# Performance work log

Measured on AMD Instinct MI355X. Metric: run time of the kernel, lower is better.

The kernel has to match this reference:

```python
import jax, jax.numpy as jnp
import numpy as np
from jax.ops import segment_sum, segment_max

N = 100000   # nodes
E = 1600000  # edges
B = 256      # graphs
H = 128      # hidden_channels
F_IN = 4     # input_size
EPS = 1e-5


def _graph_norm(x, w, b, ms, batch):
    # PyG GraphNorm: out = w * (x - ms*mean_g) / sqrt(var_g + eps) + b
    cnt = jnp.maximum(segment_sum(jnp.ones((x.shape[0],), x.dtype), batch, num_segments=B), 1.0)
    mean = segment_sum(x, batch, num_segments=B) / cnt[:, None]
    out = x - mean[batch] * ms
    var = segment_sum(out * out, batch, num_segments=B) / cnt[:, None]
    return w * out / jnp.sqrt(var + EPS)[batch] + b


def _gcn(x, W, b, src, dst):
    # GCNConv with self-loops and symmetric normalization (src/dst already include self-loops)
    h = x @ W                                              # [N, H]
    deg = segment_sum(jnp.ones_like(src, dtype=h.dtype), dst, num_segments=N)
    dinv = jax.lax.rsqrt(jnp.maximum(deg, 1.0))
    norm = dinv[src] * dinv[dst]                           # [E+N]
    return segment_sum(norm[:, None] * h[src], dst, num_segments=N) + b


def _seg_softmax(gate, batch):
    gmax = segment_max(gate, batch, num_segments=B)
    e = jnp.exp(gate - gmax[batch])
    den = segment_sum(e, batch, num_segments=B)
    return e / den[batch]


def setup_inputs() -> dict:
    key = jax.random.key(0)
    ks = jax.random.split(key, 16)
    x = jax.random.normal(ks[0], (N, F_IN), jnp.float32)
    edge_index = jax.random.randint(ks[1], (2, E), 0, N, dtype=jnp.int64)
    batch = jnp.sort(jax.random.randint(ks[2], (N,), 0, B, dtype=jnp.int64))
    r = lambda k, shp, fan: jax.random.normal(k, shp, jnp.float32) / np.sqrt(fan)
    inp = {
        "x": x, "edge_index": edge_index, "batch": batch,
        "W1": r(ks[3], (F_IN, H), F_IN), "b1": jnp.zeros((H,), jnp.float32),
        "W2": r(ks[4], (H, H), H), "b2": jnp.zeros((H,), jnp.float32),
        "W3": r(ks[5], (H, H), H), "b3": jnp.zeros((H,), jnp.float32),
        "gn0_w": jnp.ones((F_IN,), jnp.float32), "gn0_b": jnp.zeros((F_IN,), jnp.float32), "gn0_ms": jnp.ones((F_IN,), jnp.float32),
        "gn1_w": jnp.ones((H,), jnp.float32), "gn1_b": jnp.zeros((H,), jnp.float32), "gn1_ms": jnp.ones((H,), jnp.float32),
        "gn2_w": jnp.ones((H,), jnp.float32), "gn2_b": jnp.zeros((H,), jnp.float32), "gn2_ms": jnp.ones((H,), jnp.float32),
        "gn3_w": jnp.ones((H,), jnp.float32), "gn3_b": jnp.zeros((H,), jnp.float32), "gn3_ms": jnp.ones((H,), jnp.float32),
        "g1": r(ks[6], (H, H), H), "gb1": jnp.zeros((H,), jnp.float32),
        "g2": r(ks[7], (H, H), H), "gb2": jnp.zeros((H,), jnp.float32),
        "g3": r(ks[8], (H, 1), H), "gb3": jnp.zeros((1,), jnp.float32),
        "l1": r(ks[9], (H, H), H), "lb1": jnp.zeros((H,), jnp.float32),
        "l2": r(ks[10], (H, H), H), "lb2": jnp.zeros((H,), jnp.float32),
        "l3": r(ks[11], (H, 1), H), "lb3": jnp.zeros((1,), jnp.float32),
    }
    return inp


def reference(x, edge_index, batch, W1, b1, W2, b2, W3, b3,
              gn0_w, gn0_b, gn0_ms, gn1_w, gn1_b, gn1_ms,
              gn2_w, gn2_b, gn2_ms, gn3_w, gn3_b, gn3_ms,
              g1, gb1, g2, gb2, g3, gb3,
              l1, lb1, l2, lb2, l3, lb3):
    loop = jnp.arange(N, dtype=edge_index.dtype)
    src = jnp.concatenate([edge_index[0], loop])
    dst = jnp.concatenate([edge_index[1], loop])

    h = _graph_norm(x, gn0_w, gn0_b, gn0_ms, batch)
    h = _gcn(h, W1, b1, src, dst)
    h = jax.nn.relu(_graph_norm(h, gn1_w, gn1_b, gn1_ms, batch))
    h = _gcn(h, W2, b2, src, dst)
    h = jax.nn.relu(_graph_norm(h, gn2_w, gn2_b, gn2_ms, batch))
    h = _gcn(h, W3, b3, src, dst)
    h = _graph_norm(h, gn3_w, gn3_b, gn3_ms, batch)

    # GlobalAttention: gate_nn -> scalar gate per node, segment softmax, weighted sum
    g = jax.nn.relu(h @ g1 + gb1)
    g = jax.nn.relu(g @ g2 + gb2)
    gate = g @ g3 + gb3                                   # [N, 1]
    attn = _seg_softmax(gate, batch)                      # [N, 1]
    pooled = segment_sum(attn * h, batch, num_segments=B) # [B, H]

    o = jax.nn.relu(pooled @ l1 + lb1)
    o = jax.nn.relu(o @ l2 + lb2)
    return o @ l3 + lb3                                   # [B, 1]
```

## Files before the change

kernel.cpp:

```cpp
#include <hip/hip_runtime.h>
#include <hip/hip_bf16.h>

#define NN 100000
#define NE 1600000
#define NB 256
#define HD 128
#define EPS 1e-5f
#define NBUK 1563
#define EPB 8192
#define NCHK 8

typedef __attribute__((ext_vector_type(8))) short bf16x8v;
typedef __attribute__((ext_vector_type(4))) float f32x4v;

__device__ __forceinline__ float rd_dyn(const void* p, int i, int fflag) {
    if (fflag) {
        unsigned short u = ((const unsigned short*)p)[i];
        return __uint_as_float(((unsigned)u) << 16);
    }
    return ((const float*)p)[i];
}

__device__ __forceinline__ int rd_idx(const int* p, int k, int iflag) {
    return iflag ? p[k] : p[2 * k];
}

__device__ __forceinline__ unsigned short f2bf(float v) {
    __hip_bfloat16 b = __float2bfloat16(v);
    return *(unsigned short*)&b;
}

__device__ __forceinline__ float bflo(unsigned u) { return __uint_as_float(u << 16); }
__device__ __forceinline__ float bfhi(unsigned u) { return __uint_as_float(u & 0xFFFF0000u); }
__device__ __forceinline__ unsigned packbf(float a, float b) {
    return (unsigned)f2bf(a) | ((unsigned)f2bf(b) << 16);
}

__global__ void k_mark7(unsigned short* __restrict__ out, int n) {
    int i = blockIdx.x * blockDim.x + threadIdx.x;
    if (i < n) out[i] = 0x40E0;
}

__global__ void k_init(const unsigned* __restrict__ w, int* __restrict__ flags) {
    if (threadIdx.x == 0 && blockIdx.x == 0) {
        flags[0] = 0;
        flags[1] = (w[0] == 0x3F803F80u) ? 1 : 0;
    }
}

__global__ void k_detect(const int* __restrict__ w, int* __restrict__ iflag, int n) {
    int i = blockIdx.x * blockDim.x + threadIdx.x;
    if (i < n && (i & 1) && w[i] != 0) atomicOr(iflag, 1);
}

struct CvtArgs {
    const void* p[30];
    int n[30];
    int off[30];
};
__global__ void k_cvtf_all(CvtArgs a, float* __restrict__ out, const int* __restrict__ fflagp) {
    int j = blockIdx.y;
    int i = blockIdx.x * blockDim.x + threadIdx.x;
    if (i >= a.n[j]) return;
    out[a.off[j] + i] = rd_dyn(a.p[j], i, *fflagp);
}

__global__ void k_transp(const float* __restrict__ P, int o0, int o1, int o2, int o3,
                         unsigned short* __restrict__ WT) {
    int mat = blockIdx.y;
    int off = mat == 0 ? o0 : mat == 1 ? o1 : mat == 2 ? o2 : o3;
    int i = blockIdx.x * 256 + threadIdx.x;
    int nidx = i >> 7, k = i & 127;
    WT[mat * 16384 + nidx * 128 + k] = f2bf(P[off + k * 128 + nidx]);
}

__global__ void k_start(const int* __restrict__ batch, const int* __restrict__ iflagp,
                        int* __restrict__ start, int* __restrict__ batch32,
                        int* __restrict__ bcnt, int n) {
    int i = blockIdx.x * blockDim.x + threadIdx.x;
    if (i >= n) return;
    if (i < NBUK) bcnt[i] = 0;
    int ifl = *iflagp;
    int b = rd_idx(batch, i, ifl); b = b < 0 ? 0 : (b > NB - 1 ? NB - 1 : b);
    batch32[i] = b;
    int bp;
    if (i == 0) bp = -1;
    else { bp = rd_idx(batch, i - 1, ifl); bp = bp < 0 ? 0 : (bp > NB - 1 ? NB - 1 : bp); }
    for (int g = bp + 1; g <= b; ++g) start[g] = i;
    if (i == n - 1) { for (int g = b + 1; g <= NB; ++g) start[g] = n; }
}

__global__ __launch_bounds__(256) void k_bhist(const int* __restrict__ ei,
                                               const int* __restrict__ iflagp,
                                               int* __restrict__ bcnt, int e) {
    __shared__ int lh[NBUK];
    int ifl = *iflagp;
    for (int b = threadIdx.x; b < NBUK; b += 256) lh[b] = 0;
    __syncthreads();
    int s0 = blockIdx.x * EPB;
    int s1 = s0 + EPB; if (s1 > e) s1 = e;
    for (int i = s0 + threadIdx.x; i < s1; i += 256) {
        int d = rd_idx(ei, NE + i, ifl);
        int s = rd_idx(ei, i, ifl);
        if ((unsigned)d < (unsigned)NN && (unsigned)s < (unsigned)NN)
            atomicAdd(&lh[d >> 6], 1);
    }
    __syncthreads();
    for (int b = threadIdx.x; b < NBUK; b += 256)
        if (lh[b]) atomicAdd(&bcnt[b], lh[b]);
}

__global__ __launch_bounds__(1024) void k_bscan(const int* __restrict__ bcnt,
                                                int* __restrict__ boff,
                                                int* __restrict__ bcur) {
    __shared__ int part[1024];
    int t = threadIdx.x;
    int i0 = t * 2;
    int a = (i0 < NBUK) ? bcnt[i0] : 0;
    int b = (i0 + 1 < NBUK) ? bcnt[i0 + 1] : 0;
    part[t] = a + b;
    __syncthreads();
    for (int off = 1; off < 1024; off <<= 1) {
        int add = (t >= off) ? part[t - off] : 0;
        __syncthreads();
        part[t] += add;
        __syncthreads();
    }
    int base = (t > 0) ? part[t - 1] : 0;
    if (i0 < NBUK) { boff[i0] = base; bcur[i0] = base; }
    if (i0 + 1 < NBUK) { boff[i0 + 1] = base + a; bcur[i0 + 1] = base + a; }
    if (t == 1023) boff[NBUK] = part[1023];
}

__global__ __launch_bounds__(256) void k_bfill(const int* __restrict__ ei,
                                               const int* __restrict__ iflagp,
                                               int* __restrict__ bcur,
                                               unsigned* __restrict__ bkte, int e) {
    __shared__ int lh[NBUK];
    __shared__ int lbase[NBUK];
    int ifl = *iflagp;
    for (int b = threadIdx.x; b < NBUK; b += 256) lh[b] = 0;
    __syncthreads();
    int s0 = blockIdx.x * EPB;
    int s1 = s0 + EPB; if (s1 > e) s1 = e;
    for (int i = s0 + threadIdx.x; i < s1; i += 256) {
        int d = rd_idx(ei, NE + i, ifl);
        int s = rd_idx(ei, i, ifl);
        if ((unsigned)d < (unsigned)NN && (unsigned)s < (unsigned)NN)
            atomicAdd(&lh[d >> 6], 1);
    }
    __syncthreads();
    for (int b = threadIdx.x; b < NBUK; b += 256) {
        int c = lh[b];
        if (c) { lbase[b] = atomicAdd(&bcur[b], c); lh[b] = 0; }
    }
    __syncthreads();
    for (int i = s0 + threadIdx.x; i < s1; i += 256) {
        int d = rd_idx(ei, NE + i, ifl);
        int s = rd_idx(ei, i, ifl);
        if ((unsigned)d < (unsigned)NN && (unsigned)s < (unsigned)NN) {
            int b = d >> 6;
            int li = atomicAdd(&lh[b], 1);
            bkte[lbase[b] + li] = ((unsigned)s << 6) | (unsigned)(d & 63);
        }
    }
}

__global__ __launch_bounds__(256) void k_csrfin(const unsigned* __restrict__ bkte,
                                                const int* __restrict__ boff,
                                                int* __restrict__ rowptr,
                                                float* __restrict__ dinv,
                                                int* __restrict__ esrc) {
    __shared__ int lc[64];
    __shared__ int lcur[64];
    int b = blockIdx.x, t = threadIdx.x;
    int base = b * 64;
    if (t < 64) lc[t] = 0;
    __syncthreads();
    int r0 = boff[b], r1 = boff[b + 1];
    for (int j = r0 + t; j < r1; j += 256)
        atomicAdd(&lc[(int)(bkte[j] & 63u)], 1);
    __syncthreads();
    if (t < 64) {
        int v = lc[t];
        int inc = v;
#pragma unroll
        for (int off = 1; off < 64; off <<= 1) {
            int nv = __shfl_up(inc, off, 64);
            if (t >= off) inc += nv;
        }
        int ex = r0 + inc - v;
        lcur[t] = ex;
        int node = base + t;
        if (node < NN) {
            rowptr[node] = ex;
            dinv[node] = rsqrtf((float)(v + 1));
        }
    }
    if (b == NBUK - 1 && t == 0) rowptr[NN] = boff[NBUK];
    __syncthreads();
    for (int j = r0 + t; j < r1; j += 256) {
        unsigned p = bkte[j];
        int slot = atomicAdd(&lcur[p & 63u], 1);
        esrc[slot] = (int)(p >> 6);
    }
}

__global__ __launch_bounds__(64) void k_gn4(const void* __restrict__ x,
                                            const float* __restrict__ w,
                                            const float* __restrict__ bb,
                                            const float* __restrict__ ms,
                                            const int* __restrict__ start,
                                            const int* __restrict__ fflagp,
                                            float* __restrict__ out) {
    int g = blockIdx.x;
    int s0 = start[g], s1 = start[g + 1];
    if (s1 <= s0) return;
    int ff = *fflagp;
    float cnt = (float)(s1 - s0);
    int t = threadIdx.x;
    int c = t & 3, p = t >> 2;
    __shared__ float reds[64], redq[64];
    float s = 0.f, q = 0.f;
    for (int n = s0 + p; n < s1; n += 16) {
        float v = rd_dyn(x, n * 4 + c, ff);
        s += v; q = fmaf(v, v, q);
    }
    reds[t] = s; redq[t] = q; __syncthreads();
    for (int off = 8; off >= 1; off >>= 1) {
        if (p < off) { reds[t] += reds[t + 4 * off]; redq[t] += redq[t + 4 * off]; }
        __syncthreads();
    }
    float mean = reds[c] / cnt;
    float sq = redq[c] / cnt;
    float sub = mean * ms[c];
    float var = sq - 2.f * sub * mean + sub * sub;
    float scale = w[c] * rsqrtf(var + EPS);
    float bias = bb[c];
    for (int n = s0 + p; n < s1; n += 16) {
        float d = rd_dyn(x, n * 4 + c, ff) - sub;
        out[n * 4 + c] = scale * d + bias;
    }
}

__global__ __launch_bounds__(256) void k_gnstats_part(const unsigned* __restrict__ Xu,
                                                      const int* __restrict__ start,
                                                      float* __restrict__ PS,
                                                      float* __restrict__ PQ) {
    int g = blockIdx.x, k = blockIdx.y;
    int s0 = start[g], s1 = start[g + 1];
    int len = (s1 - s0 + NCHK - 1) / NCHK;
    int c0 = s0 + k * len, c1 = c0 + len; if (c1 > s1) c1 = s1;
    int t = threadIdx.x;
    int cp = t & 63, p = t >> 6;
    __shared__ float r0s[256], r1s[256], r0q[256], r1q[256];
    float s0a = 0.f, s1a = 0.f, q0a = 0.f, q1a = 0.f;
    for (int n = c0 + p; n < c1; n += 4) {
        unsigned u = Xu[n * 64 + cp];
        float lo = bflo(u), hi = bfhi(u);
        s0a += lo; q0a = fmaf(lo, lo, q0a);
        s1a += hi; q1a = fmaf(hi, hi, q1a);
    }
    r0s[t] = s0a; r1s[t] = s1a; r0q[t] = q0a; r1q[t] = q1a;
    __syncthreads();
    if (p == 0) {
        float a0 = r0s[cp] + r0s[64 + cp] + r0s[128 + cp] + r0s[192 + cp];
        float a1 = r1s[cp] + r1s[64 + cp] + r1s[128 + cp] + r1s[192 + cp];
        float b0 = r0q[cp] + r0q[64 + cp] + r0q[128 + cp] + r0q[192 + cp];
        float b1 = r1q[cp] + r1q[64 + cp] + r1q[128 + cp] + r1q[192 + cp];
        int bidx = (g * NCHK + k) * 128;
        PS[bidx + 2 * cp] = a0; PS[bidx + 2 * cp + 1] = a1;
        PQ[bidx + 2 * cp] = b0; PQ[bidx + 2 * cp + 1] = b1;
    }
}

__global__ __launch_bounds__(128) void k_gnstats_final(const float* __restrict__ PS,
                                                       const float* __restrict__ PQ,
                                                       const float* __restrict__ w,
                                                       const float* __restrict__ ms,
                                                       const int* __restrict__ start,
                                                       float* __restrict__ SUB,
                                                       float* __restrict__ SCALE) {
    int g = blockIdx.x, c = threadIdx.x;
    int n = start[g + 1] - start[g];
    if (n <= 0) return;
    float cnt = (float)n;
    float s = 0.f, q = 0.f;
#pragma unroll
    for (int k = 0; k < NCHK; ++k) {
        s += PS[(g * NCHK + k) * 128 + c];
        q += PQ[(g * NCHK + k) * 128 + c];
    }
    float mean = s / cnt;
    float sq = q / cnt;
    float sub = mean * ms[c];
    float var = sq - 2.f * sub * mean + sub * sub;
    SUB[g * 128 + c] = sub;
    SCALE[g * 128 + c] = w[c] * rsqrtf(var + EPS);
}

__global__ __launch_bounds__(256) void k_gather4(const int* __restrict__ rowptr,
                                                 const int* __restrict__ esrc,
                                                 const float* __restrict__ dinv,
                                                 const float* __restrict__ h,
                                                 float* __restrict__ out) {
    int node = blockIdx.x * blockDim.x + threadIdx.x;
    if (node >= NN) return;
    int r0 = rowptr[node], r1 = rowptr[node + 1];
    const float4* h4 = (const float4*)h;
    double ax = 0.0, ay = 0.0, az = 0.0, aw = 0.0;
    for (int j = r0; j < r1; ++j) {
        int s = esrc[j];
        float ds = dinv[s];
        float4 v = h4[s];
        ax += (double)(ds * v.x); ay += (double)(ds * v.y);
        az += (double)(ds * v.z); aw += (double)(ds * v.w);
    }
    float dd = dinv[node];
    float4 hs = h4[node];
    float4 o;
    o.x = (float)(dd * ax) + dd * dd * hs.x;
    o.y = (float)(dd * ay) + dd * dd * hs.y;
    o.z = (float)(dd * az) + dd * dd * hs.z;
    o.w = (float)(dd * aw) + dd * dd * hs.w;
    ((float4*)out)[node] = o;
}

__global__ __launch_bounds__(256) void k_gemm4b(const float* __restrict__ in,
                                                const float* __restrict__ W,
                                                const float* __restrict__ bias,
                                                unsigned short* __restrict__ out) {
    __shared__ float xs[16][4];
    int base = blockIdx.x * 16;
    int tid = threadIdx.x;
    if (tid < 64) xs[tid >> 2][tid & 3] = in[base * 4 + tid];
    __syncthreads();
    int j = tid & 127;
    int half = tid >> 7;
    float w0 = W[0 * HD + j], w1 = W[1 * HD + j], w2 = W[2 * HD + j], w3 = W[3 * HD + j];
    float bj = bias[j];
#pragma unroll
    for (int r = 0; r < 8; ++r) {
        int row = half * 8 + r;
        float v = xs[row][0] * w0 + xs[row][1] * w1 + xs[row][2] * w2 + xs[row][3] * w3 + bj;
        out[(base + row) * HD + j] = f2bf(v);
    }
}

__global__ __launch_bounds__(256) void k_gemm_mfma_bf(const unsigned* __restrict__ Xu,
                                                      const int* __restrict__ batch32,
                                                      const float* __restrict__ SUB,
                                                      const float* __restrict__ SCALE,
                                                      const float* __restrict__ gnb,
                                                      int relu,
                                                      const unsigned short* __restrict__ WT,
                                                      const float* __restrict__ dinv,
                                                      unsigned short* __restrict__ out) {
    __shared__ unsigned short xs[16][136];
    int base = blockIdx.x * 16;
    int tid = threadIdx.x;
    for (int idx = tid; idx < 1024; idx += 256) {
        int r = idx >> 6, cp = idx & 63;
        int g = batch32[base + r];
        unsigned u = Xu[(base + r) * 64 + cp];
        float2 sub = ((const float2*)(SUB + g * 128))[cp];
        float2 sc  = ((const float2*)(SCALE + g * 128))[cp];
        float2 gb  = ((const float2*)gnb)[cp];
        float va = (bflo(u) - sub.x) * sc.x + gb.x;
        float vb = (bfhi(u) - sub.y) * sc.y + gb.y;
        if (relu) { va = fmaxf(va, 0.f); vb = fmaxf(vb, 0.f); }
        xs[r][2 * cp] = f2bf(va);
        xs[r][2 * cp + 1] = f2bf(vb);
    }
    __syncthreads();
    int wave = tid >> 6, lane = tid & 63;
    int m = lane & 15, quad = lane >> 4;
    f32x4v acc0 = {0.f, 0.f, 0.f, 0.f}, acc1 = {0.f, 0.f, 0.f, 0.f};
    int c0 = wave * 32 + m, c1 = c0 + 16;
#pragma unroll
    for (int kk = 0; kk < 4; ++kk) {
        int ko = kk * 32 + quad * 8;
        bf16x8v a  = *(const bf16x8v*)&xs[m][ko];
        bf16x8v b0 = *(const bf16x8v*)&WT[c0 * 128 + ko];
        bf16x8v b1 = *(const bf16x8v*)&WT[c1 * 128 + ko];
        acc0 = __builtin_amdgcn_mfma_f32_16x16x32_bf16(a, b0, acc0, 0, 0, 0);
        acc1 = __builtin_amdgcn_mfma_f32_16x16x32_bf16(a, b1, acc1, 0, 0, 0);
    }
#pragma unroll
    for (int reg = 0; reg < 4; ++reg) {
        int row = base + quad * 4 + reg;
        float dv = dinv[row];
        out[row * 128 + c0] = f2bf(dv * acc0[reg]);
        out[row * 128 + c1] = f2bf(dv * acc1[reg]);
    }
}

__global__ __launch_bounds__(256) void k_gather_bf(const int* __restrict__ rowptr,
                                                   const int* __restrict__ esrc,
                                                   const float* __restrict__ dinv,
                                                   const unsigned* __restrict__ h,
                                                   const float* __restrict__ bias,
                                                   unsigned* __restrict__ Xu) {
    int node = blockIdx.x * 4 + (threadIdx.x >> 6);
    int lane = threadIdx.x & 63;
    if (node >= NN) return;
    int r0 = rowptr[node], r1 = rowptr[node + 1];
    double ax = 0.0, ay = 0.0;
    int j = r0;
    for (; j + 7 < r1; j += 8) {
        unsigned u[8];
#pragma unroll
        for (int q = 0; q < 8; ++q) u[q] = h[esrc[j + q] * 64 + lane];
#pragma unroll
        for (int q = 0; q < 8; ++q) {
            ax += (double)bflo(u[q]);
            ay += (double)bfhi(u[q]);
        }
    }
    for (; j < r1; ++j) {
        unsigned u = h[esrc[j] * 64 + lane];
        ax += (double)bflo(u);
        ay += (double)bfhi(u);
    }
    float dd = dinv[node];
    unsigned us = h[node * 64 + lane];
    float2 bb = ((const float2*)bias)[lane];
    float ox = dd * ((float)ax + bflo(us)) + bb.x;
    float oy = dd * ((float)ay + bfhi(us)) + bb.y;
    Xu[node * 64 + lane] = packbf(ox, oy);
}

__global__ __launch_bounds__(256) void k_gate_fused(const unsigned* __restrict__ Xu,
                                                    const int* __restrict__ batch32,
                                                    const float* __restrict__ SUB,
                                                    const float* __restrict__ SCALE,
                                                    const float* __restrict__ gnb,
                                                    const unsigned short* __restrict__ GT1,
                                                    const float* __restrict__ gb1,
                                                    const unsigned short* __restrict__ GT2,
                                                    const float* __restrict__ gb2,
                                                    const float* __restrict__ g3,
                                                    const float* __restrict__ gb3,
                                                    float* __restrict__ gate) {
    __shared__ unsigned short xs[16][136];
    __shared__ unsigned short t1[16][136];
    __shared__ float redw[64];
    int base = blockIdx.x * 16;
    int tid = threadIdx.x;
    for (int idx = tid; idx < 1024; idx += 256) {
        int r = idx >> 6, cp = idx & 63;
        int g = batch32[base + r];
        unsigned u = Xu[(base + r) * 64 + cp];
        float2 sub = ((const float2*)(SUB + g * 128))[cp];
        float2 sc  = ((const float2*)(SCALE + g * 128))[cp];
        float2 gb  = ((const float2*)gnb)[cp];
        xs[r][2 * cp] = f2bf((bflo(u) - sub.x) * sc.x + gb.x);
        xs[r][2 * cp + 1] = f2bf((bfhi(u) - sub.y) * sc.y + gb.y);
    }
    __syncthreads();
    int wave = tid >> 6, lane = tid & 63;
    int m = lane & 15, quad = lane >> 4;
    int c0 = wave * 32 + m, c1 = c0 + 16;
    f32x4v acc0 = {0.f, 0.f, 0.f, 0.f}, acc1 = {0.f, 0.f, 0.f, 0.f};
#pragma unroll
    for (int kk = 0; kk < 4; ++kk) {
        int ko = kk * 32 + quad * 8;
        bf16x8v a  = *(const bf16x8v*)&xs[m][ko];
        bf16x8v b0 = *(const bf16x8v*)&GT1[c0 * 128 + ko];
        bf16x8v b1 = *(const bf16x8v*)&GT1[c1 * 128 + ko];
        acc0 = __builtin_amdgcn_mfma_f32_16x16x32_bf16(a, b0, acc0, 0, 0, 0);
        acc1 = __builtin_amdgcn_mfma_f32_16x16x32_bf16(a, b1, acc1, 0, 0, 0);
    }
    float bj0 = gb1[c0], bj1 = gb1[c1];
#pragma unroll
    for (int reg = 0; reg < 4; ++reg) {
        int row = quad * 4 + reg;
        t1[row][c0] = f2bf(fmaxf(acc0[reg] + bj0, 0.f));
        t1[row][c1] = f2bf(fmaxf(acc1[reg] + bj1, 0.f));
    }
    __syncthreads();
    f32x4v d0 = {0.f, 0.f, 0.f, 0.f}, d1 = {0.f, 0.f, 0.f, 0.f};
#pragma unroll
    for (int kk = 0; kk < 4; ++kk) {
        int ko = kk * 32 + quad * 8;
        bf16x8v a  = *(const bf16x8v*)&t1[m][ko];
        bf16x8v b0 = *(const bf16x8v*)&GT2[c0 * 128 + ko];
        bf16x8v b1 = *(const bf16x8v*)&GT2[c1 * 128 + ko];
        d0 = __builtin_amdgcn_mfma_f32_16x16x32_bf16(a, b0, d0, 0, 0, 0);
        d1 = __builtin_amdgcn_mfma_f32_16x16x32_bf16(a, b1, d1, 0, 0, 0);
    }
    float g30 = g3[c0], g31 = g3[c1];
    float bk0 = gb2[c0], bk1 = gb2[c1];
    float contrib[4];
#pragma unroll
    for (int reg = 0; reg < 4; ++reg) {
        float v0 = fmaxf(d0[reg] + bk0, 0.f);
        float v1 = fmaxf(d1[reg] + bk1, 0.f);
        contrib[reg] = v0 * g30 + v1 * g31;
    }
#pragma unroll
    for (int mask = 1; mask <= 8; mask <<= 1) {
#pragma unroll
        for (int reg = 0; reg < 4; ++reg)
            contrib[reg] += __shfl_xor(contrib[reg], mask, 64);
    }
    if (m == 0) {
#pragma unroll
        for (int reg = 0; reg < 4; ++reg)
            redw[wave * 16 + quad * 4 + reg] = contrib[reg];
    }
    __syncthreads();
    if (tid < 16) {
        float s = redw[tid] + redw[16 + tid] + redw[32 + tid] + redw[48 + tid];
        gate[base + tid] = s + gb3[0];
    }
}

__global__ __launch_bounds__(256) void k_softmax(float* __restrict__ gate,
                                                 const int* __restrict__ start) {
    int g = blockIdx.x;
    int s0 = start[g], s1 = start[g + 1];
    if (s1 <= s0) return;
    int t = threadIdx.x;
    __shared__ float red[256];
    float m = -1e30f;
    for (int i = s0 + t; i < s1; i += 256) m = fmaxf(m, gate[i]);
    red[t] = m; __syncthreads();
    for (int off = 128; off; off >>= 1) { if (t < off) red[t] = fmaxf(red[t], red[t + off]); __syncthreads(); }
    m = red[0]; __syncthreads();
    float s = 0.f;
    for (int i = s0 + t; i < s1; i += 256) s += expf(gate[i] - m);
    red[t] = s; __syncthreads();
    for (int off = 128; off; off >>= 1) { if (t < off) red[t] += red[t + off]; __syncthreads(); }
    float inv = 1.f / red[0];
    for (int i = s0 + t; i < s1; i += 256) gate[i] = expf(gate[i] - m) * inv;
}

__global__ __launch_bounds__(256) void k_pool_part(const unsigned* __restrict__ Xu,
                                                   const float* __restrict__ SUB,
                                                   const float* __restrict__ SCALE,
                                                   const float* __restrict__ gnb,
                                                   const float* __restrict__ attn,
                                                   const int* __restrict__ start,
                                                   float* __restrict__ PP) {
    int g = blockIdx.x, k = blockIdx.y;
    int s0 = start[g], s1 = start[g + 1];
    int len = (s1 - s0 + NCHK - 1) / NCHK;
    int c0 = s0 + k * len, c1 = c0 + len; if (c1 > s1) c1 = s1;
    int t = threadIdx.x, cp = t & 63, p = t >> 6;
    __shared__ float r0s[256], r1s[256];
    float2 sub = ((const float2*)(SUB + g * 128))[cp];
    float2 sc  = ((const float2*)(SCALE + g * 128))[cp];
    float2 gb  = ((const float2*)gnb)[cp];
    float sa = 0.f, sb = 0.f;
    for (int n = c0 + p; n < c1; n += 4) {
        float a = attn[n];
        unsigned u = Xu[n * 64 + cp];
        sa += a * ((bflo(u) - sub.x) * sc.x + gb.x);
        sb += a * ((bfhi(u) - sub.y) * sc.y + gb.y);
    }
    r0s[t] = sa; r1s[t] = sb; __syncthreads();
    if (p == 0) {
        int bidx = (g * NCHK + k) * 128;
        float2 o;
        o.x = r0s[cp] + r0s[64 + cp] + r0s[128 + cp] + r0s[192 + cp];
        o.y = r1s[cp] + r1s[64 + cp] + r1s[128 + cp] + r1s[192 + cp];
        ((float2*)(PP + bidx))[cp] = o;
    }
}

__global__ __launch_bounds__(128) void k_head(const float* __restrict__ PP,
                                              const float* __restrict__ l1, const float* __restrict__ lb1,
                                              const float* __restrict__ l2, const float* __restrict__ lb2,
                                              const float* __restrict__ l3, const float* __restrict__ lb3,
                                              const int* __restrict__ fflagp,
                                              void* __restrict__ out) {
    int g = blockIdx.x, t = threadIdx.x;
    __shared__ float p[128], o[128], red[128];
    float s = 0.f;
#pragma unroll
    for (int k = 0; k < NCHK; ++k) s += PP[(g * NCHK + k) * 128 + t];
    p[t] = s; __syncthreads();
    float a = 0.f;
    for (int k = 0; k < 128; ++k) a += p[k] * l1[k * 128 + t];
    a = fmaxf(a + lb1[t], 0.f);
    o[t] = a; __syncthreads();
    float b = 0.f;
    for (int k = 0; k < 128; ++k) b += o[k] * l2[k * 128 + t];
    b = fmaxf(b + lb2[t], 0.f);
    red[t] = b * l3[t]; __syncthreads();
    for (int off = 64; off; off >>= 1) { if (t < off) red[t] += red[t + off]; __syncthreads(); }
    if (t == 0) {
        float r = red[0] + lb3[0];
        if (*fflagp) ((__hip_bfloat16*)out)[g] = __float2bfloat16(r);
        else ((float*)out)[g] = r;
    }
}

extern "C" void kernel_launch(void* const* d_in, const int* in_sizes, int n_in,
                              void* d_out, int out_size, void* d_ws, size_t ws_size,
                              hipStream_t stream) {
    const void* x = d_in[0];
    const int* ei_raw = (const int*)d_in[1];
    const int* batch_raw = (const int*)d_in[2];
    (void)n_in; (void)out_size;

    char* ws = (char*)d_ws;
    size_t off = 0;
    auto alloc = [&](size_t bytes) -> void* {
        void* p = ws + off;
        off += (bytes + 255) & ~(size_t)255;
        return p;
    };
    unsigned* Xu  = (unsigned*)alloc((size_t)NN * HD * 2);
    float* Y      = (float*)alloc((size_t)NN * HD * 4);
    float* h0     = (float*)alloc((size_t)NN * 4 * 4);
    float* z4     = (float*)alloc((size_t)NN * 4 * 4);
    float* dinv   = (float*)alloc((size_t)NN * 4);
    float* gate   = (float*)alloc((size_t)NN * 4);
    int*   start  = (int*)alloc((size_t)(NB + 1) * 4);
    int*   batch32= (int*)alloc((size_t)NN * 4);
    float* P      = (float*)alloc((size_t)131072 * 4);
    unsigned short* WT = (unsigned short*)alloc((size_t)4 * 16384 * 2);
    float* SUB    = (float*)alloc((size_t)NB * HD * 4);
    float* SCALE  = (float*)alloc((size_t)NB * HD * 4);
    float* PS     = (float*)alloc((size_t)NB * NCHK * 128 * 4);
    float* PQ     = (float*)alloc((size_t)NB * NCHK * 128 * 4);
    int*   flags  = (int*)alloc(256);
    int*   rowptr = (int*)alloc((size_t)(NN + 1) * 4);
    int*   esrc   = (int*)alloc((size_t)NE * 4);
    int*   bcnt   = (int*)alloc((size_t)NBUK * 4);
    int*   boff   = (int*)alloc((size_t)(NBUK + 1) * 4);
    int*   bcur   = (int*)alloc((size_t)NBUK * 4);
    unsigned* bkte = (unsigned*)(Y + (size_t)NN * HD / 2);
    float* PP = PS;

    if (ws_size < off) {
        k_mark7<<<1, 256, 0, stream>>>((unsigned short*)d_out, NB);
        return;
    }

    int* iflag = flags;
    int* fflag = flags + 1;
    k_init<<<1, 64, 0, stream>>>((const unsigned*)d_in[12], flags);
    k_detect<<<(NN + 255) / 256, 256, 0, stream>>>(batch_raw, iflag, NN);

    CvtArgs ca;
    float* fp[33];
    int maxn = 1;
    {
        int poff = 0;
        for (int i = 3; i < 33; ++i) {
            int n = in_sizes[i];
            ca.p[i - 3] = d_in[i];
            ca.n[i - 3] = n;
            ca.off[i - 3] = poff;
            fp[i] = P + poff;
            poff += n;
            if (n > maxn) maxn = n;
        }
    }
    {
        dim3 grid((maxn + 255) / 256, 30);
        k_cvtf_all<<<grid, 256, 0, stream>>>(ca, P, fflag);
    }
    const float *W1 = fp[3], *b1 = fp[4], *b2 = fp[6], *b3 = fp[8];
    const float *gn0w = fp[9],  *gn0b = fp[10], *gn0m = fp[11];
    const float *gn1w = fp[12], *gn1b = fp[13], *gn1m = fp[14];
    const float *gn2w = fp[15], *gn2b = fp[16], *gn2m = fp[17];
    const float *gn3w = fp[18], *gn3b = fp[19], *gn3m = fp[20];
    const float *gb1 = fp[22], *gb2 = fp[24], *g3 = fp[25], *gb3 = fp[26];
    const float *l1 = fp[27], *lb1 = fp[28], *l2 = fp[29], *lb2 = fp[30], *l3 = fp[31], *lb3 = fp[32];

    {
        dim3 grid(64, 4);
        k_transp<<<grid, 256, 0, stream>>>(P, (int)(fp[5] - P), (int)(fp[7] - P),
                                           (int)(fp[21] - P), (int)(fp[23] - P), WT);
    }
    const unsigned short* WT2 = WT;
    const unsigned short* WT3 = WT + 16384;
    const unsigned short* GT1 = WT + 2 * 16384;
    const unsigned short* GT2 = WT + 3 * 16384;

    k_start<<<(NN + 255) / 256, 256, 0, stream>>>(batch_raw, iflag, start, batch32, bcnt, NN);

    int ebg = (NE + EPB - 1) / EPB;
    k_bhist<<<ebg, 256, 0, stream>>>(ei_raw, iflag, bcnt, NE);
    k_bscan<<<1, 1024, 0, stream>>>(bcnt, boff, bcur);
    k_bfill<<<ebg, 256, 0, stream>>>(ei_raw, iflag, bcur, bkte, NE);
    k_csrfin<<<NBUK, 256, 0, stream>>>(bkte, boff, rowptr, dinv, esrc);

    k_gn4<<<NB, 64, 0, stream>>>(x, gn0w, gn0b, gn0m, start, fflag, h0);

    k_gather4<<<(NN + 255) / 256, 256, 0, stream>>>(rowptr, esrc, dinv, h0, z4);
    k_gemm4b<<<NN / 16, 256, 0, stream>>>(z4, W1, b1, (unsigned short*)Xu);

    unsigned short* Yb = (unsigned short*)Y;
    dim3 sgrid(NB, NCHK);

    k_gnstats_part<<<sgrid, 256, 0, stream>>>(Xu, start, PS, PQ);
    k_gnstats_final<<<NB, 128, 0, stream>>>(PS, PQ, gn1w, gn1m, start, SUB, SCALE);
    k_gemm_mfma_bf<<<NN / 16, 256, 0, stream>>>(Xu, batch32, SUB, SCALE, gn1b, 1, WT2, dinv, Yb);
    k_gather_bf<<<(NN + 3) / 4, 256, 0, stream>>>(rowptr, esrc, dinv, (const unsigned*)Yb, b2, Xu);

    k_gnstats_part<<<sgrid, 256, 0, stream>>>(Xu, start, PS, PQ);
    k_gnstats_final<<<NB, 128, 0, stream>>>(PS, PQ, gn2w, gn2m, start, SUB, SCALE);
    k_gemm_mfma_bf<<<NN / 16, 256, 0, stream>>>(Xu, batch32, SUB, SCALE, gn2b, 1, WT3, dinv, Yb);
    k_gather_bf<<<(NN + 3) / 4, 256, 0, stream>>>(rowptr, esrc, dinv, (const unsigned*)Yb, b3, Xu);

    k_gnstats_part<<<sgrid, 256, 0, stream>>>(Xu, start, PS, PQ);
    k_gnstats_final<<<NB, 128, 0, stream>>>(PS, PQ, gn3w, gn3m, start, SUB, SCALE);
    k_gate_fused<<<NN / 16, 256, 0, stream>>>(Xu, batch32, SUB, SCALE, gn3b,
                                              GT1, gb1, GT2, gb2, g3, gb3, gate);
    k_softmax<<<NB, 256, 0, stream>>>(gate, start);
    k_pool_part<<<sgrid, 256, 0, stream>>>(Xu, SUB, SCALE, gn3b, gate, start, PP);
    k_head<<<NB, 128, 0, stream>>>(PP, l1, lb1, l2, lb2, l3, lb3, fflag, d_out);
}
```

Baseline: 577.8 us.

## Fuse layer-1 gather with 4-wide GEMM and fold softmax normalization into pooling

After: 585.4 us. Within noise of the previous version (+1.3%).

```diff
diff --git a/kernel.cpp b/kernel.cpp
--- a/kernel.cpp
+++ b/kernel.cpp
@@ -299,52 +299,41 @@
     SCALE[g * 128 + c] = w[c] * rsqrtf(var + EPS);
 }
 
-__global__ __launch_bounds__(256) void k_gather4(const int* __restrict__ rowptr,
-                                                 const int* __restrict__ esrc,
-                                                 const float* __restrict__ dinv,
-                                                 const float* __restrict__ h,
-                                                 float* __restrict__ out) {
-    int node = blockIdx.x * blockDim.x + threadIdx.x;
+__global__ __launch_bounds__(256) void k_gather4gemm(const int* __restrict__ rowptr,
+                                                     const int* __restrict__ esrc,
+                                                     const float* __restrict__ dinv,
+                                                     const float* __restrict__ h0,
+                                                     const float* __restrict__ W1,
+                                                     const float* __restrict__ b1,
+                                                     unsigned* __restrict__ Xu) {
+    __shared__ float w1s[512];
+    __shared__ float b1s[128];
+    int tid = threadIdx.x;
+    w1s[tid] = W1[tid];
+    w1s[256 + tid] = W1[256 + tid];
+    if (tid < 128) b1s[tid] = b1[tid];
+    __syncthreads();
+    int node = blockIdx.x * 4 + (tid >> 6);
+    int lane = tid & 63;
     if (node >= NN) return;
+    int ch = lane & 3;
     int r0 = rowptr[node], r1 = rowptr[node + 1];
-    const float4* h4 = (const float4*)h;
-    double ax = 0.0, ay = 0.0, az = 0.0, aw = 0.0;
-    for (int j = r0; j < r1; ++j) {
+    double acc = 0.0;
+    for (int j = r0 + (lane >> 2); j < r1; j += 16) {
         int s = esrc[j];
-        float ds = dinv[s];
-        float4 v = h4[s];
-        ax += (double)(ds * v.x); ay += (double)(ds * v.y);
-        az += (double)(ds * v.z); aw += (double)(ds * v.w);
-    }
+        acc += (double)(dinv[s] * h0[s * 4 + ch]);
+    }
+#pragma unroll
+    for (int mask = 4; mask <= 32; mask <<= 1)
+        acc += __shfl_xor(acc, mask, 64);
     float dd = dinv[node];
-    float4 hs = h4[node];
-    float4 o;
-    o.x = (float)(dd * ax) + dd * dd * hs.x;
-    o.y = (float)(dd * ay) + dd * dd * hs.y;
-    o.z = (float)(dd * az) + dd * dd * hs.z;
-    o.w = (float)(dd * aw) + dd * dd * hs.w;
-    ((float4*)out)[node] = o;
-}
-
-__global__ __launch_bounds__(256) void k_gemm4b(const float* __restrict__ in,
-                                                const float* __restrict__ W,
-                                                const float* __restrict__ bias,
-                                                unsigned short* __restrict__ out) {
-    __shared__ float xs[16][4];
-    int base = blockIdx.x * 16;
-    int tid = threadIdx.x;
-    if (tid < 64) xs[tid >> 2][tid & 3] = in[base * 4 + tid];
-    __syncthreads();
-    int j = tid & 127;
-    int half = tid >> 7;
-    float w0 = W[0 * HD + j], w1 = W[1 * HD + j], w2 = W[2 * HD + j], w3 = W[3 * HD + j];
-    float bj = bias[j];
-#pragma unroll
-    for (int r = 0; r < 8; ++r) {
-        int row = half * 8 + r;
-        float v = xs[row][0] * w0 + xs[row][1] * w1 + xs[row][2] * w2 + xs[row][3] * w3 + bj;
-        out[(base + row) * HD + j] = f2bf(v);
-    }
+    float z = (float)(dd * acc) + dd * dd * h0[node * 4 + ch];
+    float za = __shfl(z, 0, 64), zb = __shfl(z, 1, 64);
+    float zc = __shfl(z, 2, 64), zd = __shfl(z, 3, 64);
+    int c0 = 2 * lane, c1 = 2 * lane + 1;
+    float v0 = za * w1s[c0] + zb * w1s[128 + c0] + zc * w1s[256 + c0] + zd * w1s[384 + c0] + b1s[c0];
+    float v1 = za * w1s[c1] + zb * w1s[128 + c1] + zc * w1s[256 + c1] + zd * w1s[384 + c1] + b1s[c1];
+    Xu[node * 64 + lane] = packbf(v0, v1);
 }
 
 __global__ __launch_bounds__(256) void k_gemm_mfma_bf(const unsigned* __restrict__ Xu,
@@ -516,13 +505,14 @@
     }
 }
 
-__global__ __launch_bounds__(256) void k_softmax(float* __restrict__ gate,
-                                                 const int* __restrict__ start) {
+__global__ __launch_bounds__(256) void k_smstats(const float* __restrict__ gate,
+                                                 const int* __restrict__ start,
+                                                 float2* __restrict__ SM) {
     int g = blockIdx.x;
     int s0 = start[g], s1 = start[g + 1];
-    if (s1 <= s0) return;
     int t = threadIdx.x;
     __shared__ float red[256];
+    if (s1 <= s0) { if (t == 0) SM[g] = make_float2(0.f, 1.f); return; }
     float m = -1e30f;
     for (int i = s0 + t; i < s1; i += 256) m = fmaxf(m, gate[i]);
     red[t] = m; __syncthreads();
@@ -532,15 +522,15 @@
     for (int i = s0 + t; i < s1; i += 256) s += expf(gate[i] - m);
     red[t] = s; __syncthreads();
     for (int off = 128; off; off >>= 1) { if (t < off) red[t] += red[t + off]; __syncthreads(); }
-    float inv = 1.f / red[0];
-    for (int i = s0 + t; i < s1; i += 256) gate[i] = expf(gate[i] - m) * inv;
+    if (t == 0) SM[g] = make_float2(m, red[0]);
 }
 
 __global__ __launch_bounds__(256) void k_pool_part(const unsigned* __restrict__ Xu,
                                                    const float* __restrict__ SUB,
                                                    const float* __restrict__ SCALE,
                                                    const float* __restrict__ gnb,
-                                                   const float* __restrict__ attn,
+                                                   const float* __restrict__ gate,
+                                                   const float2* __restrict__ SM,
                                                    const int* __restrict__ start,
                                                    float* __restrict__ PP) {
     int g = blockIdx.x, k = blockIdx.y;
@@ -549,12 +539,14 @@
     int c0 = s0 + k * len, c1 = c0 + len; if (c1 > s1) c1 = s1;
     int t = threadIdx.x, cp = t & 63, p = t >> 6;
     __shared__ float r0s[256], r1s[256];
+    float2 sm = SM[g];
+    float invden = 1.f / sm.y;
     float2 sub = ((const float2*)(SUB + g * 128))[cp];
     float2 sc  = ((const float2*)(SCALE + g * 128))[cp];
     float2 gb  = ((const float2*)gnb)[cp];
     float sa = 0.f, sb = 0.f;
     for (int n = c0 + p; n < c1; n += 4) {
-        float a = attn[n];
+        float a = expf(gate[n] - sm.x) * invden;
         unsigned u = Xu[n * 64 + cp];
         sa += a * ((bflo(u) - sub.x) * sc.x + gb.x);
         sb += a * ((bfhi(u) - sub.y) * sc.y + gb.y);
@@ -615,7 +607,6 @@
     unsigned* Xu  = (unsigned*)alloc((size_t)NN * HD * 2);
     float* Y      = (float*)alloc((size_t)NN * HD * 4);
     float* h0     = (float*)alloc((size_t)NN * 4 * 4);
-    float* z4     = (float*)alloc((size_t)NN * 4 * 4);
     float* dinv   = (float*)alloc((size_t)NN * 4);
     float* gate   = (float*)alloc((size_t)NN * 4);
     int*   start  = (int*)alloc((size_t)(NB + 1) * 4);
@@ -626,6 +617,7 @@
     float* SCALE  = (float*)alloc((size_t)NB * HD * 4);
     float* PS     = (float*)alloc((size_t)NB * NCHK * 128 * 4);
     float* PQ     = (float*)alloc((size_t)NB * NCHK * 128 * 4);
+    float2* SM    = (float2*)alloc((size_t)NB * 8);
     int*   flags  = (int*)alloc(256);
     int*   rowptr = (int*)alloc((size_t)(NN + 1) * 4);
     int*   esrc   = (int*)alloc((size_t)NE * 4);
@@ -692,8 +684,7 @@
 
     k_gn4<<<NB, 64, 0, stream>>>(x, gn0w, gn0b, gn0m, start, fflag, h0);
 
-    k_gather4<<<(NN + 255) / 256, 256, 0, stream>>>(rowptr, esrc, dinv, h0, z4);
-    k_gemm4b<<<NN / 16, 256, 0, stream>>>(z4, W1, b1, (unsigned short*)Xu);
+    k_gather4gemm<<<(NN + 3) / 4, 256, 0, stream>>>(rowptr, esrc, dinv, h0, W1, b1, Xu);
 
     unsigned short* Yb = (unsigned short*)Y;
     dim3 sgrid(NB, NCHK);
@@ -712,7 +703,7 @@
     k_gnstats_final<<<NB, 128, 0, stream>>>(PS, PQ, gn3w, gn3m, start, SUB, SCALE);
     k_gate_fused<<<NN / 16, 256, 0, stream>>>(Xu, batch32, SUB, SCALE, gn3b,
                                               GT1, gb1, GT2, gb2, g3, gb3, gate);
-    k_softmax<<<NB, 256, 0, stream>>>(gate, start);
-    k_pool_part<<<sgrid, 256, 0, stream>>>(Xu, SUB, SCALE, gn3b, gate, start, PP);
+    k_smstats<<<NB, 256, 0, stream>>>(gate, start, SM);
+    k_pool_part<<<sgrid, 256, 0, stream>>>(Xu, SUB, SCALE, gn3b, gate, SM, start, PP);
     k_head<<<NB, 128, 0, stream>>>(PP, l1, lb1, l2, lb2, l3, lb3, fflag, d_out);
 }
```
